# Kernel optimization log

Hardware: AMD Instinct MI355X
Metric: run time of the kernel (lower is better)

Reference implementation:

```python
import jax, jax.numpy as jnp
import numpy as np

# Gemma2-9B layer config
HID = 3584
H = 16          # query heads
KV = 8          # kv heads
G = H // KV     # GQA group size
DH = 256        # head dim
INTER = 14336
WINDOW = 1024   # sliding window size
LOGIT_CAP = 50.0
SCALING = 256.0 ** -0.5   # query_pre_attn_scalar ** -0.5
EPS = 1e-6
ROPE_BASE = 10000.0
B, S = 2, 2048


def gemma_rmsnorm(x, w, eps=EPS):
    # Gemma RMSNorm: fp32 compute, scale by (1 + w)
    xf = x.astype(jnp.float32)
    var = jnp.mean(xf * xf, axis=-1, keepdims=True)
    return (xf * jax.lax.rsqrt(var + eps) * (1.0 + w.astype(jnp.float32))).astype(x.dtype)


def apply_rope(pos, x):
    # neox-style rotary embedding; x: [B, S, n_heads, DH], pos: [B, S]
    half = DH // 2
    inv_freq = 1.0 / (ROPE_BASE ** (jnp.arange(0, half, dtype=jnp.float32) / half * 1.0))
    inv_freq = 1.0 / (ROPE_BASE ** (jnp.arange(0, DH, 2, dtype=jnp.float32) / DH))
    ang = pos.astype(jnp.float32)[..., None] * inv_freq          # [B, S, half]
    cos = jnp.cos(ang)[:, :, None, :]                            # [B, S, 1, half]
    sin = jnp.sin(ang)[:, :, None, :]
    x1, x2 = x[..., :half], x[..., half:]
    return jnp.concatenate([x1 * cos - x2 * sin, x2 * cos + x1 * sin], axis=-1).astype(x.dtype)


def setup_inputs() -> dict:
    key = jax.random.key(0)
    ks = jax.random.split(key, 12)
    s = 0.02
    inp = {
        "hidden_states": jax.random.normal(ks[0], (B, S, HID), dtype=jnp.float32),
        "positions": jnp.tile(jnp.arange(S, dtype=jnp.int32)[None, :], (B, 1)),
        "in_ln_w": jax.random.normal(ks[1], (HID,), dtype=jnp.float32) * s,
        "post_attn_ln_w": jax.random.normal(ks[2], (HID,), dtype=jnp.float32) * s,
        "pre_ff_ln_w": jax.random.normal(ks[3], (HID,), dtype=jnp.float32) * s,
        "post_ff_ln_w": jax.random.normal(ks[4], (HID,), dtype=jnp.float32) * s,
        "q_w": jax.random.normal(ks[5], (HID, H * DH), dtype=jnp.float32) * s,
        "k_w": jax.random.normal(ks[6], (HID, KV * DH), dtype=jnp.float32) * s,
        "v_w": jax.random.normal(ks[7], (HID, KV * DH), dtype=jnp.float32) * s,
        "o_w": jax.random.normal(ks[8], (H * DH, HID), dtype=jnp.float32) * s,
        "gate_w": jax.random.normal(ks[9], (HID, INTER), dtype=jnp.float32) * s,
        "up_w": jax.random.normal(ks[10], (HID, INTER), dtype=jnp.float32) * s,
        "down_w": jax.random.normal(ks[11], (INTER, HID), dtype=jnp.float32) * s,
    }
    return inp


def _decoder_layer(hidden_states, positions, in_ln_w, post_attn_ln_w, pre_ff_ln_w,
                   post_ff_ln_w, q_w, k_w, v_w, o_w, gate_w, up_w, down_w):
    # residual is None path
    residual = hidden_states
    x = gemma_rmsnorm(hidden_states, in_ln_w)

    # ---- attention ----
    q = (x @ q_w).reshape(B, S, H, DH)
    k = (x @ k_w).reshape(B, S, KV, DH)
    v = (x @ v_w).reshape(B, S, KV, DH)
    q = apply_rope(positions, q)
    k = apply_rope(positions, k)
    kv_fused = jnp.stack([k, v], axis=0)  # paged KV-cache write, modeled densely

    qg = q.reshape(B, S, KV, G, DH)
    # scores: [B, KV, G, S(q), S(k)]
    scores = jnp.einsum('bsngd,btnd->bngst', qg, k) * SCALING
    scores = LOGIT_CAP * jnp.tanh(scores / LOGIT_CAP)  # logit softcapping
    i = jnp.arange(S)[:, None]
    j = jnp.arange(S)[None, :]
    mask = (j <= i) & (i - j < WINDOW)                 # causal + sliding window
    scores = jnp.where(mask, scores, jnp.finfo(scores.dtype).min)
    probs = jax.nn.softmax(scores, axis=-1)
    attn = jnp.einsum('bngst,btnd->bsngd', probs, v).reshape(B, S, H * DH)
    attn_out = attn @ o_w

    x = gemma_rmsnorm(attn_out, post_attn_ln_w)
    x = residual + x
    residual = x

    # ---- GeGLU MLP ----
    x = gemma_rmsnorm(x, pre_ff_ln_w)
    inter = (x @ up_w) * jax.nn.gelu(x @ gate_w)
    x = inter @ down_w
    x = gemma_rmsnorm(x, post_ff_ln_w)
    return x, residual, kv_fused


def reference(hidden_states, positions, in_ln_w, post_attn_ln_w, pre_ff_ln_w,
              post_ff_ln_w, q_w, k_w, v_w, o_w, gate_w, up_w, down_w):
    return _decoder_layer(hidden_states, positions, in_ln_w, post_attn_ln_w,
                          pre_ff_ln_w, post_ff_ln_w, q_w, k_w, v_w, o_w,
                          gate_w, up_w, down_w)
```

## Files before the change

kernel.cpp:

```cpp
#include <hip/hip_runtime.h>
#include <stdint.h>

typedef unsigned short ushortT;
typedef float f32x4 __attribute__((ext_vector_type(4)));
typedef short short8 __attribute__((ext_vector_type(8)));

#define HID 3584
#define NH 16
#define NKV 8
#define DH 256
#define SEQ 2048
#define NB 2
#define NTOK 4096
#define INTERDIM 14336
#define ICH 7168
#define WINDOW 1024

__device__ __forceinline__ ushortT f2bf(float x) {
  union { float f; uint32_t u; } v; v.f = x;
  uint32_t r = v.u + 0x7fffu + ((v.u >> 16) & 1u);
  return (ushortT)(r >> 16);
}
__device__ __forceinline__ float bf2f(uint32_t b) {
  union { uint32_t u; float f; } v; v.u = b << 16;
  return v.f;
}
__device__ __forceinline__ void gll16(const void* g, void* l) {
  __builtin_amdgcn_global_load_lds((const __attribute__((address_space(1))) void*)g,
                                   (__attribute__((address_space(3))) void*)l, 16, 0, 0);
}
__device__ __forceinline__ void sbar() {
  asm volatile("" ::: "memory");
  __builtin_amdgcn_s_barrier();
  asm volatile("" ::: "memory");
}

__global__ __launch_bounds__(256) void transpose_cvt(const float* __restrict__ in,
                                                     ushortT* __restrict__ out,
                                                     int in_rs, int out_rs) {
  __shared__ float tile[64][65];
  const int r0 = blockIdx.y * 64, c0 = blockIdx.x * 64;
  const int t = threadIdx.x, tc = (t & 15) * 4, tr = t >> 4;
#pragma unroll
  for (int p = 0; p < 4; ++p) {
    int r = tr + p * 16;
    float4 v = *(const float4*)&in[(size_t)(r0 + r) * in_rs + c0 + tc];
    tile[r][tc] = v.x; tile[r][tc + 1] = v.y; tile[r][tc + 2] = v.z; tile[r][tc + 3] = v.w;
  }
  __syncthreads();
#pragma unroll
  for (int p = 0; p < 4; ++p) {
    int r = tr + p * 16;
    ushort4 u;
    u.x = f2bf(tile[tc + 0][r]); u.y = f2bf(tile[tc + 1][r]);
    u.z = f2bf(tile[tc + 2][r]); u.w = f2bf(tile[tc + 3][r]);
    *(ushort4*)&out[(size_t)(c0 + r) * out_rs + r0 + tc] = u;
  }
}

__global__ __launch_bounds__(256) void vtrans(const float* __restrict__ vsrc,
                                              ushortT* __restrict__ vT) {
  __shared__ float tile[64][65];
  const int z = blockIdx.z, b = z >> 3, n = z & 7;
  const float* in = vsrc + (size_t)b * SEQ * (NKV * DH) + n * DH;
  ushortT* out = vT + (size_t)z * DH * SEQ;
  const int s0 = blockIdx.y * 64, d0 = blockIdx.x * 64;
  const int t = threadIdx.x, tc = (t & 15) * 4, tr = t >> 4;
#pragma unroll
  for (int p = 0; p < 4; ++p) {
    int r = tr + p * 16;
    float4 v = *(const float4*)&in[(size_t)(s0 + r) * (NKV * DH) + d0 + tc];
    tile[r][tc] = v.x; tile[r][tc + 1] = v.y; tile[r][tc + 2] = v.z; tile[r][tc + 3] = v.w;
  }
  __syncthreads();
#pragma unroll
  for (int p = 0; p < 4; ++p) {
    int r = tr + p * 16;
    ushort4 u;
    u.x = f2bf(tile[tc + 0][r]); u.y = f2bf(tile[tc + 1][r]);
    u.z = f2bf(tile[tc + 2][r]); u.w = f2bf(tile[tc + 3][r]);
    *(ushort4*)&out[(size_t)(d0 + r) * SEQ + s0 + tc] = u;
  }
}

__device__ __forceinline__ float block_sum448(float v, float* sb) {
#pragma unroll
  for (int o = 32; o; o >>= 1) v += __shfl_xor(v, o, 64);
  __syncthreads();
  if ((threadIdx.x & 63) == 0) sb[threadIdx.x >> 6] = v;
  __syncthreads();
  float s = 0.f;
#pragma unroll
  for (int i = 0; i < 7; ++i) s += sb[i];
  return s;
}

__global__ __launch_bounds__(448) void rms_in(const float* __restrict__ in,
                                              const float* __restrict__ w,
                                              ushortT* __restrict__ out) {
  __shared__ float sb[8];
  const size_t row = blockIdx.x;
  const int c = threadIdx.x * 8;
  const float* p = in + row * HID + c;
  float4 a = *(const float4*)p, bq = *(const float4*)(p + 4);
  float v[8] = {a.x, a.y, a.z, a.w, bq.x, bq.y, bq.z, bq.w};
  float ssq = 0.f;
#pragma unroll
  for (int j = 0; j < 8; ++j) ssq += v[j] * v[j];
  float s = block_sum448(ssq, sb);
  float rs = rsqrtf(s * (1.0f / HID) + 1e-6f);
  uint32_t o[4];
#pragma unroll
  for (int j = 0; j < 4; ++j) {
    float r0 = v[2 * j] * rs * (1.f + w[c + 2 * j]);
    float r1 = v[2 * j + 1] * rs * (1.f + w[c + 2 * j + 1]);
    o[j] = (uint32_t)f2bf(r0) | ((uint32_t)f2bf(r1) << 16);
  }
  *(uint4*)(out + row * HID + c) = make_uint4(o[0], o[1], o[2], o[3]);
}

__global__ __launch_bounds__(448) void rms_add(const float* ao,
                                               const float* __restrict__ h,
                                               const float* __restrict__ w1,
                                               const float* __restrict__ w2,
                                               float* resid,
                                               ushortT* __restrict__ x2) {
  __shared__ float sb[8];
  const size_t row = blockIdx.x;
  const int c = threadIdx.x * 8;
  const float* p = ao + row * HID + c;
  float4 a = *(const float4*)p, bq = *(const float4*)(p + 4);
  float v[8] = {a.x, a.y, a.z, a.w, bq.x, bq.y, bq.z, bq.w};
  float ssq = 0.f;
#pragma unroll
  for (int j = 0; j < 8; ++j) ssq += v[j] * v[j];
  float s1 = block_sum448(ssq, sb);
  float rs1 = rsqrtf(s1 * (1.0f / HID) + 1e-6f);
  const float* hp = h + row * HID + c;
  float4 h0 = *(const float4*)hp, h1 = *(const float4*)(hp + 4);
  float hv[8] = {h0.x, h0.y, h0.z, h0.w, h1.x, h1.y, h1.z, h1.w};
  float r[8];
  float ssq2 = 0.f;
#pragma unroll
  for (int j = 0; j < 8; ++j) {
    r[j] = hv[j] + v[j] * rs1 * (1.f + w1[c + j]);
    ssq2 += r[j] * r[j];
  }
  float* rp = resid + row * HID + c;
  *(float4*)rp = make_float4(r[0], r[1], r[2], r[3]);
  *(float4*)(rp + 4) = make_float4(r[4], r[5], r[6], r[7]);
  float s2 = block_sum448(ssq2, sb);
  float rs2 = rsqrtf(s2 * (1.0f / HID) + 1e-6f);
  uint32_t o[4];
#pragma unroll
  for (int j = 0; j < 4; ++j) {
    float q0 = r[2 * j] * rs2 * (1.f + w2[c + 2 * j]);
    float q1 = r[2 * j + 1] * rs2 * (1.f + w2[c + 2 * j + 1]);
    o[j] = (uint32_t)f2bf(q0) | ((uint32_t)f2bf(q1) << 16);
  }
  *(uint4*)(x2 + row * HID + c) = make_uint4(o[0], o[1], o[2], o[3]);
}

__global__ __launch_bounds__(448) void rms_out(const float* in,
                                               const float* __restrict__ w,
                                               float* out) {
  __shared__ float sb[8];
  const size_t row = blockIdx.x;
  const int c = threadIdx.x * 8;
  const float* p = in + row * HID + c;
  float4 a = *(const float4*)p, bq = *(const float4*)(p + 4);
  float v[8] = {a.x, a.y, a.z, a.w, bq.x, bq.y, bq.z, bq.w};
  float ssq = 0.f;
#pragma unroll
  for (int j = 0; j < 8; ++j) ssq += v[j] * v[j];
  float s = block_sum448(ssq, sb);
  float rs = rsqrtf(s * (1.0f / HID) + 1e-6f);
  float* op = out + row * HID + c;
  float r[8];
#pragma unroll
  for (int j = 0; j < 8; ++j) r[j] = v[j] * rs * (1.f + w[c + j]);
  *(float4*)op = make_float4(r[0], r[1], r[2], r[3]);
  *(float4*)(op + 4) = make_float4(r[4], r[5], r[6], r[7]);
}

__global__ __launch_bounds__(128) void rope_q_k(const ushortT* __restrict__ qraw,
                                                const int* __restrict__ pos,
                                                ushortT* __restrict__ qr) {
  const int s = blockIdx.x, h = blockIdx.y, b = blockIdx.z, i = threadIdx.x;
  float p = (float)pos[b * SEQ + s];
  float ang = p * exp2f(-(float)i * (13.287712379549449f / 128.f));
  float sn, cs;
  sincosf(ang, &sn, &cs);
  size_t ib = ((size_t)b * SEQ + s) * (NH * DH) + (size_t)h * DH + i;
  float x1 = bf2f(qraw[ib]), x2 = bf2f(qraw[ib + 128]);
  size_t ob = (((size_t)b * NH + h) * SEQ + s) * DH + i;
  qr[ob] = f2bf(x1 * cs - x2 * sn);
  qr[ob + 128] = f2bf(x2 * cs + x1 * sn);
}

__global__ __launch_bounds__(128) void rope_k_k(const ushortT* __restrict__ kraw,
                                                const int* __restrict__ pos,
                                                ushortT* __restrict__ kr,
                                                float* __restrict__ kv0) {
  const int s = blockIdx.x, n = blockIdx.y, b = blockIdx.z, i = threadIdx.x;
  float p = (float)pos[b * SEQ + s];
  float ang = p * exp2f(-(float)i * (13.287712379549449f / 128.f));
  float sn, cs;
  sincosf(ang, &sn, &cs);
  size_t ib = ((size_t)b * SEQ + s) * (NKV * DH) + (size_t)n * DH + i;
  float x1 = bf2f(kraw[ib]), x2 = bf2f(kraw[ib + 128]);
  float o1 = x1 * cs - x2 * sn, o2 = x2 * cs + x1 * sn;
  size_t ob = (((size_t)b * NKV + n) * SEQ + s) * DH + i;
  kr[ob] = f2bf(o1);
  kr[ob + 128] = f2bf(o2);
  size_t kb = (((size_t)b * SEQ + s) * NKV + n) * DH + i;
  kv0[kb] = o1;
  kv0[kb + 128] = o2;
}

template <int OUTMODE>
__global__ __launch_bounds__(512) void gemm8p(const ushortT* __restrict__ A, int lda,
                                              const ushortT* __restrict__ Bt, int ldb,
                                              void* __restrict__ C, int N, int K) {
  __shared__ ushortT lds[65536];
  char* lb = (char*)lds;
  const int tid = threadIdx.x;
  const int nwg = gridDim.x * gridDim.y;
  const int lin = blockIdx.y * gridDim.x + blockIdx.x;
  const int cpx = nwg >> 3;
  const int lin2 = (lin & 7) * cpx + (lin >> 3);
  const int bx = lin2 % gridDim.x, by = lin2 / gridDim.x;
  const int m0 = by * 256, n0 = bx * 256;
  const int l = tid & 63, lr = l & 15, lg = l >> 4;
  const int wid = tid >> 6, wm = wid >> 2, wn = wid & 3;
  const int sr = tid >> 3, sc = tid & 7;

  f32x4 acc[8][4];
#pragma unroll
  for (int i = 0; i < 8; ++i)
#pragma unroll
    for (int j = 0; j < 4; ++j) acc[i][j] = (f32x4){0.f, 0.f, 0.f, 0.f};

  const int nt = K >> 6;
  const ushortT* Ag = A + (size_t)m0 * lda;
  const ushortT* Bg = Bt + (size_t)n0 * ldb;

  auto stHT = [&](int tt, int op, int h) {
    char* dst = lb + (tt & 1) * 65536 + op * 32768 + h * 16384;
    const ushortT* g = (op ? Bg : Ag) + (size_t)tt * 64;
    const int ld = op ? ldb : lda;
#pragma unroll
    for (int L = 0; L < 2; ++L) {
      int row = h * 128 + L * 64 + sr;
      gll16((const char*)(g + (size_t)row * ld) + ((sc ^ (row & 7)) << 4),
            dst + L * 8192 + tid * 16);
    }
  };
  short8 afA[4][2], bfA[2][2], bfB[2][2];
  auto rdA = [&](const char* buf, int mh) {
#pragma unroll
    for (int i4 = 0; i4 < 4; ++i4) {
      int r = wm * 128 + mh * 64 + i4 * 16 + lr;
      const char* base = buf + wm * 16384 + (r & 127) * 128;
#pragma unroll
      for (int ks = 0; ks < 2; ++ks)
        afA[i4][ks] = *(const short8*)(base + (((ks * 4 + lg) ^ (r & 7)) << 4));
    }
  };
  auto rdB = [&](const char* buf, int nh, short8 (*bf)[2]) {
#pragma unroll
    for (int j = 0; j < 2; ++j) {
      int r = wn * 64 + nh * 32 + j * 16 + lr;
      const char* base = buf + 32768 + (wn >> 1) * 16384 + (r & 127) * 128;
#pragma unroll
      for (int ks = 0; ks < 2; ++ks)
        bf[j][ks] = *(const short8*)(base + (((ks * 4 + lg) ^ (r & 7)) << 4));
    }
  };
  auto mid = [&]() {
    sbar();
    asm volatile("s_waitcnt lgkmcnt(0)" ::: "memory");
    __builtin_amdgcn_sched_barrier(0);
  };
  auto mm = [&](int mh, int nh, short8 (*bf)[2]) {
    __builtin_amdgcn_s_setprio(1);
#pragma unroll
    for (int i4 = 0; i4 < 4; ++i4)
#pragma unroll
      for (int j = 0; j < 2; ++j)
#pragma unroll
        for (int ks = 0; ks < 2; ++ks)
          acc[mh * 4 + i4][nh * 2 + j] = __builtin_amdgcn_mfma_f32_16x16x32_bf16(
              afA[i4][ks], bf[j][ks], acc[mh * 4 + i4][nh * 2 + j], 0, 0, 0);
    __builtin_amdgcn_s_setprio(0);
  };

  stHT(0, 0, 0); stHT(0, 0, 1); stHT(0, 1, 0); stHT(0, 1, 1);
  stHT(1, 0, 0); stHT(1, 0, 1); stHT(1, 1, 0); stHT(1, 1, 1);
  asm volatile("s_waitcnt vmcnt(8)" ::: "memory");
  sbar();

  const int nit = nt >> 1;
  const char* b0 = lb;
  const char* b1 = lb + 65536;
  for (int i = 0; i < nit; ++i) {
    const int t1 = 2 * i + 1, s0 = 2 * i + 2, s1 = 2 * i + 3;
    const bool hs0 = s0 < nt, hs1 = s1 < nt, pre = i > 0;
    rdA(b0, 0);
    rdB(b0, 0, bfA);
    if (pre) stHT(t1, 0, 1);
    asm volatile("s_waitcnt lgkmcnt(8)" ::: "memory");
    mid(); mm(0, 0, bfA); sbar();
    rdB(b0, 1, bfB);
    if (pre) stHT(t1, 1, 1);
    mid(); mm(0, 1, bfB); sbar();
    rdA(b0, 1);
    if (hs0) stHT(s0, 1, 0);
    mid(); mm(1, 0, bfA); sbar();
    if (hs0) stHT(s0, 0, 0);
    mid(); mm(1, 1, bfB);
    if (hs0) asm volatile("s_waitcnt vmcnt(4)" ::: "memory");
    else     asm volatile("s_waitcnt vmcnt(0)" ::: "memory");
    sbar();
    rdA(b1, 0);
    rdB(b1, 0, bfA);
    if (hs0) stHT(s0, 0, 1);
    asm volatile("s_waitcnt lgkmcnt(8)" ::: "memory");
    mid(); mm(0, 0, bfA); sbar();
    rdB(b1, 1, bfB);
    if (hs0) stHT(s0, 1, 1);
    mid(); mm(0, 1, bfB); sbar();
    rdA(b1, 1);
    if (hs1) stHT(s1, 1, 0);
    mid(); mm(1, 0, bfA); sbar();
    if (hs1) stHT(s1, 0, 0);
    mid(); mm(1, 1, bfB);
    if (hs1) asm volatile("s_waitcnt vmcnt(4)" ::: "memory");
    sbar();
  }
#pragma unroll
  for (int mi = 0; mi < 8; ++mi)
#pragma unroll
    for (int nj = 0; nj < 4; ++nj)
#pragma unroll
      for (int r = 0; r < 4; ++r) {
        size_t row = (size_t)(m0 + wm * 128 + mi * 16 + lg * 4 + r);
        size_t col = (size_t)(n0 + wn * 64 + nj * 16 + lr);
        size_t idx = row * N + col;
        if (OUTMODE == 0)
          ((float*)C)[idx] = acc[mi][nj][r];
        else if (OUTMODE == 1)
          ((ushortT*)C)[idx] = f2bf(acc[mi][nj][r]);
        else
          ((float*)C)[idx] += acc[mi][nj][r];
      }
}

__global__ __launch_bounds__(256) void swiglu_k(const ushortT* __restrict__ g,
                                                const ushortT* __restrict__ u,
                                                ushortT* __restrict__ o, int n16) {
  int i = blockIdx.x * 256 + threadIdx.x;
  if (i >= n16) return;
  uint4 gv = ((const uint4*)g)[i];
  uint4 uv = ((const uint4*)u)[i];
  uint32_t ga[4] = {gv.x, gv.y, gv.z, gv.w};
  uint32_t ua[4] = {uv.x, uv.y, uv.z, uv.w};
  uint32_t rr[4];
#pragma unroll
  for (int j = 0; j < 4; ++j) {
    float g0 = bf2f(ga[j] & 0xffffu), g1 = bf2f(ga[j] >> 16);
    float u0 = bf2f(ua[j] & 0xffffu), u1 = bf2f(ua[j] >> 16);
    float e0 = 0.5f * g0 * (1.f + tanhf(0.7978845608f * (g0 + 0.044715f * g0 * g0 * g0)));
    float e1 = 0.5f * g1 * (1.f + tanhf(0.7978845608f * (g1 + 0.044715f * g1 * g1 * g1)));
    rr[j] = (uint32_t)f2bf(u0 * e0) | ((uint32_t)f2bf(u1 * e1) << 16);
  }
  ((uint4*)o)[i] = make_uint4(rr[0], rr[1], rr[2], rr[3]);
}

__global__ __launch_bounds__(256) void attn_fwd(const ushortT* __restrict__ Q,
                                                const ushortT* __restrict__ Kk,
                                                const ushortT* __restrict__ Vt,
                                                ushortT* __restrict__ Out) {
  __shared__ ushortT Kl[32 * 256];
  __shared__ ushortT Vl[256 * 32];
  __shared__ ushortT Pl[4][16 * 32];
  const int tid = threadIdx.x;
  const int w = tid >> 6, l = tid & 63, lr = l & 15, lg = l >> 4;
  const int h = blockIdx.y, b = blockIdx.z;
  const int n = h >> 1;
  const int qs = blockIdx.x * 64;
  const int sw = qs + w * 16;

  const ushortT* qp = Q + (((size_t)b * NH + h) * SEQ + (sw + lr)) * DH;
  short8 qf[8];
#pragma unroll
  for (int kk = 0; kk < 8; ++kk) qf[kk] = *(const short8*)(qp + kk * 32 + lg * 8);

  f32x4 acc[16];
#pragma unroll
  for (int i = 0; i < 16; ++i) acc[i] = (f32x4){0.f, 0.f, 0.f, 0.f};
  float m_s = -1e30f, l_s = 0.f;

  const ushortT* Kbase = Kk + ((size_t)b * NKV + n) * SEQ * DH;
  const ushortT* Vbase = Vt + ((size_t)b * NKV + n) * DH * SEQ;

  int tlo = qs - (WINDOW - 1);
  if (tlo < 0) tlo = 0;
  const int t0b = tlo & ~31;
  const int nt = (qs + 64 - t0b) >> 5;
  const int scol = sw + lr;

  for (int it = 0; it < nt; ++it) {
    const int t0 = t0b + it * 32;
    __syncthreads();
    {
      const int rowk = tid >> 5;
      const int cbk = (tid & 31) * 16;
#pragma unroll
      for (int c = 0; c < 4; ++c) {
        int row = c * 8 + rowk;
        int cbs = cbk ^ ((row & 7) << 4);
        gll16((const char*)(Kbase + (size_t)(t0 + row) * DH) + cbs, (char*)Kl + c * 4096 + tid * 16);
      }
      const int rowv = tid >> 2;
      const int cbv = (tid & 3) * 16;
#pragma unroll
      for (int c = 0; c < 4; ++c) {
        int row = c * 64 + rowv;
        int cbs = cbv ^ ((row & 3) << 4);
        gll16((const char*)(Vbase + (size_t)row * SEQ + t0) + cbs, (char*)Vl + c * 4096 + tid * 16);
      }
    }
    __syncthreads();
    f32x4 st[2];
#pragma unroll
    for (int tt = 0; tt < 2; ++tt) {
      f32x4 a = (f32x4){0.f, 0.f, 0.f, 0.f};
      const int krow = tt * 16 + lr;
      const char* kb = (const char*)Kl + krow * 512;
      const int swz = (krow & 7) << 4;
#pragma unroll
      for (int kk = 0; kk < 8; ++kk) {
        short8 kf = *(const short8*)(kb + ((kk * 64 + lg * 16) ^ swz));
        a = __builtin_amdgcn_mfma_f32_16x16x32_bf16(kf, qf[kk], a, 0, 0, 0);
      }
      st[tt] = a;
    }
    float pvv[8];
    float tmax = -1e30f;
#pragma unroll
    for (int tt = 0; tt < 2; ++tt)
#pragma unroll
      for (int r = 0; r < 4; ++r) {
        int t = t0 + tt * 16 + lg * 4 + r;
        float x = st[tt][r] * 0.0625f;
        x = 50.f * tanhf(x * 0.02f);
        bool ok = (t <= scol) && (scol - t < WINDOW);
        x = ok ? x : -1e30f;
        pvv[tt * 4 + r] = x;
        tmax = fmaxf(tmax, x);
      }
    tmax = fmaxf(tmax, __shfl_xor(tmax, 16, 64));
    tmax = fmaxf(tmax, __shfl_xor(tmax, 32, 64));
    float mnew = fmaxf(m_s, tmax);
    float fsc = __expf(m_s - mnew);
    m_s = mnew;
    float tsum = 0.f;
#pragma unroll
    for (int i = 0; i < 8; ++i) {
      pvv[i] = __expf(pvv[i] - mnew);
      tsum += pvv[i];
    }
    tsum += __shfl_xor(tsum, 16, 64);
    tsum += __shfl_xor(tsum, 32, 64);
    l_s = l_s * fsc + tsum;
    {
      char* pb = (char*)&Pl[w][0] + lr * 64;
      const int pswz = (lr & 3) << 4;
#pragma unroll
      for (int tt = 0; tt < 2; ++tt) {
        uint32_t p01 = (uint32_t)f2bf(pvv[tt * 4 + 0]) | ((uint32_t)f2bf(pvv[tt * 4 + 1]) << 16);
        uint32_t p23 = (uint32_t)f2bf(pvv[tt * 4 + 2]) | ((uint32_t)f2bf(pvv[tt * 4 + 3]) << 16);
        *(uint32_t*)(pb + ((tt * 32 + lg * 8 + 0) ^ pswz)) = p01;
        *(uint32_t*)(pb + ((tt * 32 + lg * 8 + 4) ^ pswz)) = p23;
      }
    }
    float fr[4];
#pragma unroll
    for (int r = 0; r < 4; ++r) fr[r] = __shfl(fsc, lg * 4 + r, 64);
#pragma unroll
    for (int nd = 0; nd < 16; ++nd) {
      acc[nd][0] *= fr[0]; acc[nd][1] *= fr[1];
      acc[nd][2] *= fr[2]; acc[nd][3] *= fr[3];
    }
    const char* pfb = (const char*)&Pl[w][0] + lr * 64;
    short8 pf = *(const short8*)(pfb + ((lg * 16) ^ ((lr & 3) << 4)));
#pragma unroll
    for (int nd = 0; nd < 16; ++nd) {
      const int vrow = nd * 16 + lr;
      short8 vf = *(const short8*)((const char*)Vl + vrow * 64 + ((lg * 16) ^ ((vrow & 3) << 4)));
      acc[nd] = __builtin_amdgcn_mfma_f32_16x16x32_bf16(pf, vf, acc[nd], 0, 0, 0);
    }
  }
  float linv[4];
#pragma unroll
  for (int r = 0; r < 4; ++r) linv[r] = 1.f / __shfl(l_s, lg * 4 + r, 64);
#pragma unroll
  for (int nd = 0; nd < 16; ++nd)
#pragma unroll
    for (int r = 0; r < 4; ++r) {
      size_t row = (size_t)b * SEQ + sw + lg * 4 + r;
      Out[row * (NH * DH) + (size_t)h * DH + nd * 16 + lr] = f2bf(acc[nd][r] * linv[r]);
    }
}

extern "C" void kernel_launch(void* const* d_in, const int* in_sizes, int n_in,
                              void* d_out, int out_size, void* d_ws, size_t ws_size,
                              hipStream_t stream) {
  const float* hs = (const float*)d_in[0];
  const int* pos = (const int*)d_in[1];
  const float* w_in = (const float*)d_in[2];
  const float* w_pa = (const float*)d_in[3];
  const float* w_pf = (const float*)d_in[4];
  const float* w_po = (const float*)d_in[5];
  const float* qw = (const float*)d_in[6];
  const float* kw = (const float*)d_in[7];
  const float* vw = (const float*)d_in[8];
  const float* ow = (const float*)d_in[9];
  const float* gw = (const float*)d_in[10];
  const float* uw = (const float*)d_in[11];
  const float* dw = (const float*)d_in[12];

  float* out_x = (float*)d_out;
  float* out_res = out_x + (size_t)NTOK * HID;
  float* out_kv0 = out_res + (size_t)NTOK * HID;
  float* out_kv1 = out_kv0 + (size_t)NTOK * NKV * DH;

  char* ws = (char*)d_ws;
  char* W = ws;
  ushortT* qwT = (ushortT*)(W);
  ushortT* kwT = (ushortT*)(W + 29360128);
  ushortT* vwT = (ushortT*)(W + 29360128 + 14680064);
  ushortT* owT = (ushortT*)(W + 29360128 + 2 * 14680064);
  ushortT* wS0 = (ushortT*)(W);
  ushortT* wS1 = (ushortT*)(W + 51380224);
  char* R = ws + 102760448;
  ushortT* x1 = (ushortT*)(R);
  ushortT* qraw_b = (ushortT*)(R + 29360128);
  ushortT* kraw_b = (ushortT*)(R + 62914560);
  ushortT* qrope = (ushortT*)(R + 79691776);
  ushortT* krope = (ushortT*)(R + 113246208);
  ushortT* vT = (ushortT*)(R + 130023424);
  ushortT* attnb = qraw_b;
  ushortT* x2 = x1;
  ushortT* gateC = (ushortT*)(R + 29360128);
  ushortT* upC = (ushortT*)(R + 29360128 + 58720256);
  ushortT* interC = gateC;
  float* attn_out = out_res;

  transpose_cvt<<<dim3(4096 / 64, HID / 64), 256, 0, stream>>>(qw, qwT, 4096, HID);
  transpose_cvt<<<dim3(2048 / 64, HID / 64), 256, 0, stream>>>(kw, kwT, 2048, HID);
  transpose_cvt<<<dim3(2048 / 64, HID / 64), 256, 0, stream>>>(vw, vwT, 2048, HID);
  transpose_cvt<<<dim3(HID / 64, 4096 / 64), 256, 0, stream>>>(ow, owT, HID, 4096);

  rms_in<<<NTOK, 448, 0, stream>>>(hs, w_in, x1);

  gemm8p<1><<<dim3(16, 16), 512, 0, stream>>>(x1, HID, qwT, HID, qraw_b, 4096, HID);
  gemm8p<1><<<dim3(8, 16), 512, 0, stream>>>(x1, HID, kwT, HID, kraw_b, 2048, HID);
  gemm8p<0><<<dim3(8, 16), 512, 0, stream>>>(x1, HID, vwT, HID, out_kv1, 2048, HID);

  rope_q_k<<<dim3(SEQ, NH, NB), 128, 0, stream>>>(qraw_b, pos, qrope);
  rope_k_k<<<dim3(SEQ, NKV, NB), 128, 0, stream>>>(kraw_b, pos, krope, out_kv0);
  vtrans<<<dim3(DH / 64, SEQ / 64, NB * NKV), 256, 0, stream>>>(out_kv1, vT);

  attn_fwd<<<dim3(SEQ / 64, NH, NB), 256, 0, stream>>>(qrope, krope, vT, attnb);

  gemm8p<0><<<dim3(HID / 256, 16), 512, 0, stream>>>(attnb, 4096, owT, 4096, attn_out, HID, 4096);

  rms_add<<<NTOK, 448, 0, stream>>>(attn_out, hs, w_pa, w_pf, out_res, x2);

  for (int c = 0; c < 2; ++c) {
    transpose_cvt<<<dim3(ICH / 64, HID / 64), 256, 0, stream>>>(gw + (size_t)c * ICH, wS0,
                                                                INTERDIM, HID);
    gemm8p<1><<<dim3(ICH / 256, 16), 512, 0, stream>>>(x2, HID, wS0, HID, gateC, ICH, HID);
    transpose_cvt<<<dim3(ICH / 64, HID / 64), 256, 0, stream>>>(uw + (size_t)c * ICH, wS1,
                                                                INTERDIM, HID);
    gemm8p<1><<<dim3(ICH / 256, 16), 512, 0, stream>>>(x2, HID, wS1, HID, upC, ICH, HID);
    int n16 = (int)((size_t)NTOK * ICH / 8);
    swiglu_k<<<(n16 + 255) / 256, 256, 0, stream>>>(gateC, upC, interC, n16);
    transpose_cvt<<<dim3(HID / 64, ICH / 64), 256, 0, stream>>>(dw + (size_t)c * ICH * HID, wS0,
                                                                HID, ICH);
    if (c == 0)
      gemm8p<0><<<dim3(HID / 256, 16), 512, 0, stream>>>(interC, ICH, wS0, ICH, out_x, HID, ICH);
    else
      gemm8p<2><<<dim3(HID / 256, 16), 512, 0, stream>>>(interC, ICH, wS0, ICH, out_x, HID, ICH);
  }

  rms_out<<<NTOK, 448, 0, stream>>>(out_x, w_po, out_x);
}
```

Baseline: 2.190 ms.

## Double-buffer A fragments and software-pipeline LDS reads with MFMA in GEMM loop

Result: slower. 4.659 ms (+112.7%).

```diff
diff --git a/kernel.cpp b/kernel.cpp
--- a/kernel.cpp
+++ b/kernel.cpp
@@ -256,15 +256,15 @@
             dst + L * 8192 + tid * 16);
     }
   };
-  short8 afA[4][2], bfA[2][2], bfB[2][2];
-  auto rdA = [&](const char* buf, int mh) {
+  short8 afA[4][2], afB[4][2], bfA[2][2], bfB[2][2];
+  auto rdA = [&](const char* buf, int mh, short8 (*af)[2]) {
 #pragma unroll
     for (int i4 = 0; i4 < 4; ++i4) {
       int r = wm * 128 + mh * 64 + i4 * 16 + lr;
       const char* base = buf + wm * 16384 + (r & 127) * 128;
 #pragma unroll
       for (int ks = 0; ks < 2; ++ks)
-        afA[i4][ks] = *(const short8*)(base + (((ks * 4 + lg) ^ (r & 7)) << 4));
+        af[i4][ks] = *(const short8*)(base + (((ks * 4 + lg) ^ (r & 7)) << 4));
     }
   };
   auto rdB = [&](const char* buf, int nh, short8 (*bf)[2]) {
@@ -277,12 +277,8 @@
         bf[j][ks] = *(const short8*)(base + (((ks * 4 + lg) ^ (r & 7)) << 4));
     }
   };
-  auto mid = [&]() {
-    sbar();
-    asm volatile("s_waitcnt lgkmcnt(0)" ::: "memory");
+  auto mm = [&](int mh, int nh, short8 (*af)[2], short8 (*bf)[2]) {
     __builtin_amdgcn_sched_barrier(0);
-  };
-  auto mm = [&](int mh, int nh, short8 (*bf)[2]) {
     __builtin_amdgcn_s_setprio(1);
 #pragma unroll
     for (int i4 = 0; i4 < 4; ++i4)
@@ -291,52 +287,68 @@
 #pragma unroll
         for (int ks = 0; ks < 2; ++ks)
           acc[mh * 4 + i4][nh * 2 + j] = __builtin_amdgcn_mfma_f32_16x16x32_bf16(
-              afA[i4][ks], bf[j][ks], acc[mh * 4 + i4][nh * 2 + j], 0, 0, 0);
+              af[i4][ks], bf[j][ks], acc[mh * 4 + i4][nh * 2 + j], 0, 0, 0);
     __builtin_amdgcn_s_setprio(0);
   };
 
-  stHT(0, 0, 0); stHT(0, 0, 1); stHT(0, 1, 0); stHT(0, 1, 1);
-  stHT(1, 0, 0); stHT(1, 0, 1); stHT(1, 1, 0); stHT(1, 1, 1);
+  stHT(0, 0, 0); stHT(0, 1, 0); stHT(0, 1, 1); stHT(0, 0, 1);
+  stHT(1, 0, 0); stHT(1, 1, 0); stHT(1, 1, 1); stHT(1, 0, 1);
   asm volatile("s_waitcnt vmcnt(8)" ::: "memory");
   sbar();
+  rdA(lb, 0, afA);
+  rdB(lb, 0, bfA);
 
   const int nit = nt >> 1;
   const char* b0 = lb;
   const char* b1 = lb + 65536;
   for (int i = 0; i < nit; ++i) {
-    const int t1 = 2 * i + 1, s0 = 2 * i + 2, s1 = 2 * i + 3;
-    const bool hs0 = s0 < nt, hs1 = s1 < nt, pre = i > 0;
-    rdA(b0, 0);
-    rdB(b0, 0, bfA);
-    if (pre) stHT(t1, 0, 1);
+    const int s0 = 2 * i + 2, s1 = 2 * i + 3;
+    const bool hs0 = s0 < nt, hs1 = s1 < nt, nxt = i + 1 < nit;
+    sbar();
+    rdB(b0, 1, bfB);
+    asm volatile("s_waitcnt lgkmcnt(4)" ::: "memory");
+    mm(0, 0, afA, bfA);
+    sbar();
+    rdA(b0, 1, afB);
+    if (hs0) stHT(s0, 0, 0);
     asm volatile("s_waitcnt lgkmcnt(8)" ::: "memory");
-    mid(); mm(0, 0, bfA); sbar();
-    rdB(b0, 1, bfB);
-    if (pre) stHT(t1, 1, 1);
-    mid(); mm(0, 1, bfB); sbar();
-    rdA(b0, 1);
+    mm(0, 1, afA, bfB);
+    sbar();
     if (hs0) stHT(s0, 1, 0);
-    mid(); mm(1, 0, bfA); sbar();
-    if (hs0) stHT(s0, 0, 0);
-    mid(); mm(1, 1, bfB);
+    asm volatile("s_waitcnt lgkmcnt(0)" ::: "memory");
+    mm(1, 0, afB, bfA);
     if (hs0) asm volatile("s_waitcnt vmcnt(4)" ::: "memory");
     else     asm volatile("s_waitcnt vmcnt(0)" ::: "memory");
     sbar();
-    rdA(b1, 0);
+    rdA(b1, 0, afA);
     rdB(b1, 0, bfA);
-    if (hs0) stHT(s0, 0, 1);
+    if (hs0) { stHT(s0, 1, 1); stHT(s0, 0, 1); }
+    asm volatile("s_waitcnt lgkmcnt(12)" ::: "memory");
+    mm(1, 1, afB, bfB);
+    sbar();
+    rdB(b1, 1, bfB);
+    asm volatile("s_waitcnt lgkmcnt(4)" ::: "memory");
+    mm(0, 0, afA, bfA);
+    sbar();
+    rdA(b1, 1, afB);
+    if (hs1) stHT(s1, 0, 0);
     asm volatile("s_waitcnt lgkmcnt(8)" ::: "memory");
-    mid(); mm(0, 0, bfA); sbar();
-    rdB(b1, 1, bfB);
-    if (hs0) stHT(s0, 1, 1);
-    mid(); mm(0, 1, bfB); sbar();
-    rdA(b1, 1);
+    mm(0, 1, afA, bfB);
+    sbar();
     if (hs1) stHT(s1, 1, 0);
-    mid(); mm(1, 0, bfA); sbar();
-    if (hs1) stHT(s1, 0, 0);
-    mid(); mm(1, 1, bfB);
-    if (hs1) asm volatile("s_waitcnt vmcnt(4)" ::: "memory");
-    sbar();
+    asm volatile("s_waitcnt lgkmcnt(0)" ::: "memory");
+    mm(1, 0, afB, bfA);
+    if (hs1)      asm volatile("s_waitcnt vmcnt(4)" ::: "memory");
+    else if (hs0) asm volatile("s_waitcnt vmcnt(0)" ::: "memory");
+    sbar();
+    if (nxt) {
+      rdA(b0, 0, afA);
+      rdB(b0, 0, bfA);
+    }
+    if (hs1) { stHT(s1, 1, 1); stHT(s1, 0, 1); }
+    if (nxt) asm volatile("s_waitcnt lgkmcnt(12)" ::: "memory");
+    else     asm volatile("s_waitcnt lgkmcnt(0)" ::: "memory");
+    mm(1, 1, afB, bfB);
   }
 #pragma unroll
   for (int mi = 0; mi < 8; ++mi)
```
